# Kernel optimization log

Hardware: AMD Instinct MI355X
Metric: run time of the kernel (lower is better)

The kernel has to match this reference:

```python
import jax, jax.numpy as jnp
import numpy as np

B, T, N, D, H, MH = 4, 16, 128, 16, 64, 128  # batch, timesteps, nodes, n_in_node, n_hid, msg_hid


def setup_inputs() -> dict:
    key = jax.random.key(0)
    ks = jax.random.split(key, 24)
    s = 0.1
    inp = {
        'A': jax.random.uniform(ks[0], (B, N, N), dtype=jnp.float32),
        'X': jax.random.normal(ks[1], (B, T, N, D), dtype=jnp.float32),
        'W_msg1': s * jax.random.normal(ks[2], (2 * H, MH), dtype=jnp.float32),
        'b_msg1': s * jax.random.normal(ks[3], (MH,), dtype=jnp.float32),
        'W_msg2': s * jax.random.normal(ks[4], (MH, H), dtype=jnp.float32),
        'b_msg2': s * jax.random.normal(ks[5], (H,), dtype=jnp.float32),
        'W_ir': s * jax.random.normal(ks[6], (D, H), dtype=jnp.float32),
        'b_ir': s * jax.random.normal(ks[7], (H,), dtype=jnp.float32),
        'W_ii': s * jax.random.normal(ks[8], (D, H), dtype=jnp.float32),
        'b_ii': s * jax.random.normal(ks[9], (H,), dtype=jnp.float32),
        'W_in': s * jax.random.normal(ks[10], (D, H), dtype=jnp.float32),
        'b_in': s * jax.random.normal(ks[11], (H,), dtype=jnp.float32),
        'W_hr': s * jax.random.normal(ks[12], (H, H), dtype=jnp.float32),
        'W_hi': s * jax.random.normal(ks[13], (H, H), dtype=jnp.float32),
        'W_hh': s * jax.random.normal(ks[14], (H, H), dtype=jnp.float32),
        'W_o1': s * jax.random.normal(ks[15], (H, H), dtype=jnp.float32),
        'b_o1': s * jax.random.normal(ks[16], (H,), dtype=jnp.float32),
        'W_o2': s * jax.random.normal(ks[17], (H, H), dtype=jnp.float32),
        'b_o2': s * jax.random.normal(ks[18], (H,), dtype=jnp.float32),
        'W_o3': s * jax.random.normal(ks[19], (H, D), dtype=jnp.float32),
        'b_o3': s * jax.random.normal(ks[20], (D,), dtype=jnp.float32),
        'log_sigma': jnp.log(jnp.float32(0.1)),
    }
    return inp


def reference(A, X, W_msg1, b_msg1, W_msg2, b_msg2, W_ir, b_ir, W_ii, b_ii,
              W_in, b_in, W_hr, W_hi, W_hh, W_o1, b_o1, W_o2, b_o2, W_o3,
              b_o3, log_sigma):
    Bv, Tv, Nv, Dv = X.shape
    Hv = W_hr.shape[0]
    # project_adjacency: symmetrize, zero diag, clamp to [0,1]
    A = (A + jnp.swapaxes(A, -1, -2)) * 0.5
    A = A * (1.0 - jnp.eye(Nv, dtype=A.dtype))
    A = jnp.clip(A, 0.0, 1.0)
    # split msg_fc1 into sender / receiver halves (cat([senders, receivers]) @ W)
    W1s, W1r = W_msg1[:Hv], W_msg1[Hv:]

    def step(carry, xs):
        hidden, total = carry
        x_t, x_next = xs  # [B,N,D]
        # message passing on hidden state: msg1[b,i,j] = tanh(h_i@W1s + h_j@W1r + b)
        hs = hidden @ W1s                      # [B,N,MH] sender part
        hr = hidden @ W1r + b_msg1             # [B,N,MH] receiver part
        m1 = jnp.tanh(hs[:, :, None, :] + hr[:, None, :, :])  # [B,N,N,MH]
        msg = jnp.tanh(m1 @ W_msg2 + b_msg2)   # [B,N,N,H]
        # weight by soft adjacency, sum over senders i -> agg at receiver j
        agg = jnp.einsum('bij,bijh->bjh', A, msg)  # [B,N,H]
        # GRU-style gating
        r = jax.nn.sigmoid(x_t @ W_ir + b_ir + agg @ W_hr)
        i = jax.nn.sigmoid(x_t @ W_ii + b_ii + agg @ W_hi)
        n = jnp.tanh(x_t @ W_in + b_in + r * (agg @ W_hh))
        hidden_new = (1.0 - i) * n + i * hidden
        # output MLP with residual
        p1 = jax.nn.relu(hidden_new @ W_o1 + b_o1)
        p2 = jax.nn.relu(p1 @ W_o2 + b_o2)
        pred = x_t + (p2 @ W_o3 + b_o3)
        # gaussian log-likelihood
        sigma = jnp.exp(log_sigma)
        mse = jnp.sum((x_next - pred) ** 2)
        const = Nv * Dv * Bv * jnp.log(sigma * jnp.sqrt(2.0 * jnp.pi))
        total = total - (mse / (2.0 * sigma ** 2) + const)
        return (hidden_new, total), pred

    hidden0 = jnp.zeros((Bv, Nv, Hv), dtype=X.dtype)
    xs = (jnp.swapaxes(X[:, :-1], 0, 1), jnp.swapaxes(X[:, 1:], 0, 1))  # time-major
    (_, loglik), preds = jax.lax.scan(step, (hidden0, jnp.float32(0.0)), xs)
    X_pred = jnp.swapaxes(preds, 0, 1)  # [B, T-1, N, D]
    return X_pred, loglik
```

## Files before the change

kernel.cpp:

```cpp
#include <hip/hip_runtime.h>

#define NBLK 512
#define CSCALE 2.8853900817779268f

#define OFF_HS   0
#define OFF_PART 65536
#define OFF_SYNC 66048
#define OFF_BF   85248

#define SYNC_ROOT 15360
#define SYNC_FLAG 17280

#define BW2F  0
#define BWIR  8192
#define BWII  9216
#define BWIN  10240
#define BWHR  11264
#define BWHI  15360
#define BWHH  19456
#define BWO1  23552
#define BWO2  27648
#define BWO3  31744
#define BW1S  32768
#define BW1RT 49152

#define INIT_TOTAL (32768 + 19200 + 49152 + 8192)

typedef __attribute__((ext_vector_type(8))) __bf16 bf16x8;
typedef __attribute__((ext_vector_type(4))) float f32x4;
union frag_u { bf16x8 v; unsigned short s[8]; int4 q; };
union ldu { int4 q; unsigned short s[8]; unsigned u[4]; };

__device__ __forceinline__ unsigned short f2b(float x) {
  unsigned int u = __float_as_uint(x);
  u += 0x7fffu + ((u >> 16) & 1u);
  return (unsigned short)(u >> 16);
}
__device__ __forceinline__ float b2f(unsigned short u) {
  return __uint_as_float(((unsigned int)u) << 16);
}
__device__ __forceinline__ float fast_tanh(float x) {
  float e = __builtin_amdgcn_exp2f(x * CSCALE);
  return 1.0f - 2.0f * __builtin_amdgcn_rcpf(e + 1.0f);
}
__device__ __forceinline__ float tanh_pre(float x) {
  float e = __builtin_amdgcn_exp2f(x);
  return 1.0f - 2.0f * __builtin_amdgcn_rcpf(e + 1.0f);
}
__device__ __forceinline__ float fast_sigmoid(float x) {
  float e = __builtin_amdgcn_exp2f(x * -1.4426950408889634f);
  return __builtin_amdgcn_rcpf(1.0f + e);
}
__device__ __forceinline__ unsigned pack_bf2(float lo, float hi) {
  unsigned a = __float_as_uint(lo) + 0x8000u;
  unsigned b = __float_as_uint(hi) + 0x8000u;
  return __builtin_amdgcn_perm(b, a, 0x07060302u);
}
__device__ __forceinline__ void st_coh_u32(unsigned* p, unsigned v) {
  __hip_atomic_store(p, v, __ATOMIC_RELAXED, __HIP_MEMORY_SCOPE_AGENT);
}

__global__ void init_kernel(const float* __restrict__ W_msg2,
                            const float* __restrict__ W_ir, const float* __restrict__ W_ii,
                            const float* __restrict__ W_in,
                            const float* __restrict__ W_hr, const float* __restrict__ W_hi,
                            const float* __restrict__ W_hh,
                            const float* __restrict__ W_o1, const float* __restrict__ W_o2,
                            const float* __restrict__ W_o3,
                            const float* __restrict__ W_msg1, float* __restrict__ ws) {
  int idx = blockIdx.x * 256 + threadIdx.x;
  unsigned short* bw = (unsigned short*)(ws + OFF_BF);
  if (idx < 32768) { ws[OFF_HS + idx] = 0.0f; return; }
  idx -= 32768;
  if (idx < 19200) { ((int*)(ws + OFF_SYNC))[idx] = 0; return; }
  idx -= 19200;
  if (idx < 8192) {
    int f = idx >> 9, l = (idx >> 3) & 63, jj = idx & 7;
    int kc = f >> 2, nt = f & 3;
    int k = kc * 32 + ((l >> 4) << 3) + jj;
    int n = (nt << 4) + (l & 15);
    bw[BW2F + idx] = f2b(W_msg2[k * 64 + n] * CSCALE);
    return;
  }
  idx -= 8192;
  if (idx < 1024) { bw[BWIR + idx] = f2b(W_ir[idx]); return; }
  idx -= 1024;
  if (idx < 1024) { bw[BWII + idx] = f2b(W_ii[idx]); return; }
  idx -= 1024;
  if (idx < 1024) { bw[BWIN + idx] = f2b(W_in[idx]); return; }
  idx -= 1024;
  if (idx < 4096) { bw[BWHR + idx] = f2b(W_hr[idx]); return; }
  idx -= 4096;
  if (idx < 4096) { bw[BWHI + idx] = f2b(W_hi[idx]); return; }
  idx -= 4096;
  if (idx < 4096) { bw[BWHH + idx] = f2b(W_hh[idx]); return; }
  idx -= 4096;
  if (idx < 4096) { bw[BWO1 + idx] = f2b(W_o1[idx]); return; }
  idx -= 4096;
  if (idx < 4096) { bw[BWO2 + idx] = f2b(W_o2[idx]); return; }
  idx -= 4096;
  if (idx < 1024) { bw[BWO3 + idx] = f2b(W_o3[idx]); return; }
  idx -= 1024;
  if (idx < 16384) { bw[BW1S + idx] = f2b(W_msg1[idx]); return; }
  idx -= 16384;
  if (idx < 8192) {
    int m = idx >> 6, h = idx & 63;
    bw[BW1RT + idx] = f2b(W_msg1[(64 + h) * 128 + m]);
    return;
  }
}

__launch_bounds__(512, 4)
__global__ void step_all_kernel(const float* __restrict__ A, const float* __restrict__ X,
                                const float* __restrict__ b_msg1, const float* __restrict__ b_msg2,
                                const float* __restrict__ b_ir, const float* __restrict__ b_ii,
                                const float* __restrict__ b_in,
                                const float* __restrict__ b_o1, const float* __restrict__ b_o2,
                                const float* __restrict__ b_o3,
                                float* __restrict__ ws, float* __restrict__ out) {
  const int tid = threadIdx.x;
  const int bj = blockIdx.x;
  const int b = (bj >> 6) & 3;
  const int j = (bj & 63) | ((bj >> 8) << 6);
  const int row = (b << 7) + j;
  const int wave = tid >> 6, lane = tid & 63;
  const unsigned short* bw = (const unsigned short*)(ws + OFF_BF);
  unsigned short* hs16 = (unsigned short*)(ws + OFF_HS);
  int* sync = (int*)(ws + OFF_SYNC);

  __shared__ __align__(16) unsigned short lds_bf[8192];
  __shared__ __align__(16) unsigned short lds_gate_t[12288];
  __shared__ __align__(16) unsigned short lds_w1t[8192];
  __shared__ __align__(16) unsigned short lds_xw[3072];
  __shared__ __align__(16) float sh_hr[128];
  __shared__ __align__(16) float sh_Ar[128];
  __shared__ __align__(16) float sh_aggw[8][64];
  __shared__ __align__(16) float sh_agg[64];
  __shared__ __align__(16) float sh_xall[256];
  __shared__ __align__(16) float sh_hid[64];
  __shared__ __align__(16) float sh_hist[960];
  __shared__ __align__(16) float sh_pre[8][64];
  __shared__ int sh_w01;

  {
    const int4* src = (const int4*)bw;
    int4* dst = (int4*)lds_bf;
    for (int i = tid; i < 1024; i += 512) dst[i] = src[i];
  }
  for (int i = tid; i < 12288; i += 512) {
    int g = i >> 12, r = i & 4095, c = r >> 8, rem = r & 255, h = rem >> 2, s = rem & 3;
    lds_gate_t[i] = bw[BWHR + (g << 12) + (((c << 2) + s) << 6) + h];
  }
  for (int i = tid; i < 8192; i += 512) {
    int c = i >> 9, rem = i & 511, m = rem >> 2, s = rem & 3;
    lds_w1t[i] = bw[BW1S + (((c << 2) + s) << 7) + m];
  }
  for (int i = tid; i < 3072; i += 512) lds_xw[i] = bw[BWIR + i];
  if (tid < 256) {
    int t0 = tid >> 4, d = tid & 15;
    sh_xall[tid] = X[(((b << 4) + t0) << 11) + (j << 4) + d];
  }
  if (tid < 128) {
    float a1 = A[(b << 14) + (j << 7) + tid];
    float a2 = A[(b << 14) + (tid << 7) + j];
    float v = 0.5f * (a1 + a2);
    v = (tid == j) ? 0.0f : v;
    sh_Ar[tid] = fminf(fmaxf(v, 0.0f), 1.0f);
    sh_hr[tid] = b_msg1[tid] * CSCALE;
  } else if (tid < 192) {
    sh_hid[tid - 128] = 0.0f;
  }
  if (tid == 0) sh_w01 = 0;

  float b2v[4];
#pragma unroll
  for (int nt = 0; nt < 4; ++nt) b2v[nt] = b_msg2[nt * 16 + (lane & 15)] * CSCALE;
  float my_bias = 0.0f;
  if (wave == 0) my_bias = b_ir[lane];
  else if (wave == 1) my_bias = b_ii[lane];
  else if (wave == 3) my_bias = b_in[lane];
  const float bm1a = b_msg1[lane], bm1b = b_msg1[lane + 64];
  const float bo1 = b_o1[lane], bo2 = b_o2[lane];
  const float bo3 = (lane < 16) ? b_o3[lane] : 0.0f;
  float macc = 0.0f;

  const int lane15 = lane & 15;
  const int k0 = (lane >> 4) << 3;
  __syncthreads();

  for (int t = 0; t < 15; ++t) {
    const int par = t & 1;
    const unsigned short* hs_cur = hs16 + par * 65536;
    unsigned short* hs_nxt = hs16 + (par ^ 1) * 65536;

    ldu va[4];
    {
      const unsigned short* p0 = hs_cur + (((b << 7) + (wave << 4) + lane15) << 7) + k0;
      asm volatile(
          "global_load_dwordx4 %0, %4, off sc0 sc1\n\t"
          "global_load_dwordx4 %1, %4, off offset:64 sc0 sc1\n\t"
          "global_load_dwordx4 %2, %4, off offset:128 sc0 sc1\n\t"
          "global_load_dwordx4 %3, %4, off offset:192 sc0 sc1\n\t"
          "s_waitcnt vmcnt(0)"
          : "=&v"(va[0].q), "=&v"(va[1].q), "=&v"(va[2].q), "=&v"(va[3].q)
          : "v"(p0)
          : "memory");
    }

    float part[4] = {0.f, 0.f, 0.f, 0.f};
    {
      f32x4 acc[4];
#pragma unroll
      for (int nt = 0; nt < 4; ++nt) acc[nt] = (f32x4){0.f, 0.f, 0.f, 0.f};
#pragma unroll
      for (int kc = 0; kc < 4; ++kc) {
        const ldu& u = va[kc];
        const float* hp = sh_hr + kc * 32 + k0;
        frag_u Af;
        int* ap = (int*)&Af.q;
#pragma unroll
        for (int p = 0; p < 4; ++p) {
          unsigned w = u.u[p];
          float x0 = __uint_as_float(w << 16) + hp[2 * p];
          float x1 = __uint_as_float(w & 0xffff0000u) + hp[2 * p + 1];
          ap[p] = (int)pack_bf2(tanh_pre(x0), tanh_pre(x1));
        }
#pragma unroll
        for (int nt = 0; nt < 4; ++nt) {
          frag_u Bfr;
          Bfr.q = *(((const int4*)lds_bf) + (((kc << 2) + nt) << 6) + lane);
          acc[nt] = __builtin_amdgcn_mfma_f32_16x16x32_bf16(Af.v, Bfr.v, acc[nt], 0, 0, 0);
        }
      }
      const int ibase = wave << 4;
      float4 aw = *(const float4*)(sh_Ar + ibase + ((lane >> 4) << 2));
#pragma unroll
      for (int r = 0; r < 4; ++r) {
        float wv = (r == 0) ? aw.x : (r == 1) ? aw.y : (r == 2) ? aw.z : aw.w;
#pragma unroll
        for (int nt = 0; nt < 4; ++nt)
          part[nt] += wv * tanh_pre(acc[nt][r] + b2v[nt]);
      }
    }
#pragma unroll
    for (int nt = 0; nt < 4; ++nt) {
      part[nt] += __shfl_xor(part[nt], 16);
      part[nt] += __shfl_xor(part[nt], 32);
    }
    if (lane < 16) {
#pragma unroll
      for (int nt = 0; nt < 4; ++nt) sh_aggw[wave][nt * 16 + lane] = part[nt];
    }
    __syncthreads();
    if (tid < 64) {
      float s = 0.0f;
#pragma unroll
      for (int w = 0; w < 8; ++w) s += sh_aggw[w][tid];
      sh_agg[tid] = s;
    }
    __syncthreads();

    if (wave < 4) {
      float s = 0.0f;
      if (wave != 2) {
        s = my_bias;
        const int g = (wave == 3) ? 2 : wave;
        const float* xr = sh_xall + (t << 4);
#pragma unroll
        for (int d = 0; d < 16; ++d) s += xr[d] * b2f(lds_xw[(g << 10) + (d << 6) + lane]);
      }
      if (wave != 3) {
        const ushort4* gp = ((const ushort4*)lds_gate_t) + (wave << 10) + lane;
        const float4* ag = (const float4*)sh_agg;
        float a0 = s, a1 = 0.f, a2 = 0.f, a3 = 0.f;
#pragma unroll
        for (int c = 0; c < 16; ++c) {
          ushort4 wv = gp[c << 6];
          float4 av = ag[c];
          a0 += av.x * b2f(wv.x); a1 += av.y * b2f(wv.y);
          a2 += av.z * b2f(wv.z); a3 += av.w * b2f(wv.w);
        }
        s = (a0 + a1) + (a2 + a3);
      }
      sh_pre[wave][lane] = s;
    }
    __syncthreads();
    if (tid < 64) {
      float r  = fast_sigmoid(sh_pre[0][tid]);
      float ig = fast_sigmoid(sh_pre[1][tid]);
      float n  = fast_tanh(sh_pre[3][tid] + r * sh_pre[2][tid]);
      float hnew = (1.0f - ig) * n + ig * sh_hid[tid];
      sh_hid[tid] = hnew;
      sh_hist[t * 64 + tid] = hnew;
    }
    __syncthreads();

    if (t < 14) {
      if (wave <= 1) {
        const int m = tid;
        const ushort4* wp = ((const ushort4*)lds_w1t) + m;
        const float4* h4 = (const float4*)sh_hid;
        float a0 = 0.f, a1 = 0.f, a2 = 0.f, a3 = 0.f;
#pragma unroll
        for (int c = 0; c < 16; ++c) {
          ushort4 wv = wp[c << 7];
          float4 hv = h4[c];
          a0 += hv.x * b2f(wv.x); a1 += hv.y * b2f(wv.y);
          a2 += hv.z * b2f(wv.z); a3 += hv.w * b2f(wv.w);
        }
        float s = ((a0 + a1) + (a2 + a3)) * CSCALE;
        float hi = __shfl_down(s, 1);
        if (!(lane & 1))
          st_coh_u32((unsigned*)hs_nxt + (row << 6) + (m >> 1), pack_bf2(s, hi));
        asm volatile("s_waitcnt vmcnt(0)" ::: "memory");
        if (lane == 0) atomicAdd(&sh_w01, 1);
        if (wave == 0 && lane == 0) {
          const int tgt = t + 1;
          while (__hip_atomic_load(&sh_w01, __ATOMIC_RELAXED, __HIP_MEMORY_SCOPE_WORKGROUP) < 2 * tgt) {}
          const int bt = b * 15 + t;
          int* leaf = sync + ((bt << 3) + (j & 7)) * 32;
          int* root = sync + SYNC_ROOT + bt * 32;
          int* flag = sync + SYNC_FLAG + bt * 32;
          int r = __hip_atomic_fetch_add(leaf, 1, __ATOMIC_RELAXED, __HIP_MEMORY_SCOPE_AGENT);
          if (r == 15) {
            int r2 = __hip_atomic_fetch_add(root, 1, __ATOMIC_RELAXED, __HIP_MEMORY_SCOPE_AGENT);
            if (r2 == 7)
              __hip_atomic_store(flag, 1, __ATOMIC_RELAXED, __HIP_MEMORY_SCOPE_AGENT);
          }
          while (__hip_atomic_load(flag, __ATOMIC_RELAXED, __HIP_MEMORY_SCOPE_AGENT) == 0)
            __builtin_amdgcn_s_sleep(1);
        }
      } else if (wave == 2) {
        const int4* wp1 = (const int4*)(bw + BW1RT + (lane << 6));
        const int4* wp2 = (const int4*)(bw + BW1RT + ((lane + 64) << 6));
        const float4* h4 = (const float4*)sh_hid;
        float s1a = bm1a, s1b = 0.f, s2a = bm1b, s2b = 0.f;
#pragma unroll
        for (int c = 0; c < 8; ++c) {
          ldu u1, u2; u1.q = wp1[c]; u2.q = wp2[c];
          float4 h0 = h4[2 * c], h1 = h4[2 * c + 1];
          s1a += h0.x * b2f(u1.s[0]); s1b += h0.y * b2f(u1.s[1]);
          s1a += h0.z * b2f(u1.s[2]); s1b += h0.w * b2f(u1.s[3]);
          s1a += h1.x * b2f(u1.s[4]); s1b += h1.y * b2f(u1.s[5]);
          s1a += h1.z * b2f(u1.s[6]); s1b += h1.w * b2f(u1.s[7]);
          s2a += h0.x * b2f(u2.s[0]); s2b += h0.y * b2f(u2.s[1]);
          s2a += h0.z * b2f(u2.s[2]); s2b += h0.w * b2f(u2.s[3]);
          s2a += h1.x * b2f(u2.s[4]); s2b += h1.y * b2f(u2.s[5]);
          s2a += h1.z * b2f(u2.s[6]); s2b += h1.w * b2f(u2.s[7]);
        }
        sh_hr[lane] = (s1a + s1b) * CSCALE;
        sh_hr[lane + 64] = (s2a + s2b) * CSCALE;
      }
    }
    __syncthreads();
  }

  for (int i = tid; i < 8192; i += 512) {
    int o = i >> 12, r = i & 4095, c = r >> 8, rem = r & 255, h = rem >> 2, s = rem & 3;
    lds_gate_t[i] = bw[BWO1 + (o << 12) + (((c << 2) + s) << 6) + h];
  }
  for (int i = tid; i < 1024; i += 512) {
    int c = i >> 6, rem = i & 63, d = rem >> 2, s = rem & 3;
    lds_gate_t[8192 + i] = bw[BWO3 + (((c << 2) + s) << 4) + d];
  }
  __syncthreads();

#pragma unroll
  for (int it = 0; it < 2; ++it) {
    const int tt = wave + (it << 3);
    if (tt >= 15) continue;
    const float4* h4 = (const float4*)(sh_hist + tt * 64);
    {
      const ushort4* r1 = ((const ushort4*)lds_gate_t) + lane;
      float a0 = bo1, a1 = 0.f, a2 = 0.f, a3 = 0.f;
#pragma unroll
      for (int c = 0; c < 16; ++c) {
        ushort4 wv = r1[c << 6]; float4 hv = h4[c];
        a0 += hv.x * b2f(wv.x); a1 += hv.y * b2f(wv.y);
        a2 += hv.z * b2f(wv.z); a3 += hv.w * b2f(wv.w);
      }
      sh_pre[wave][lane] = fmaxf((a0 + a1) + (a2 + a3), 0.0f);
    }
    {
      const ushort4* r2 = ((const ushort4*)lds_gate_t) + 1024 + lane;
      const float4* p4 = (const float4*)sh_pre[wave];
      float a0 = bo2, a1 = 0.f, a2 = 0.f, a3 = 0.f;
#pragma unroll
      for (int c = 0; c < 16; ++c) {
        ushort4 wv = r2[c << 6]; float4 pv = p4[c];
        a0 += pv.x * b2f(wv.x); a1 += pv.y * b2f(wv.y);
        a2 += pv.z * b2f(wv.z); a3 += pv.w * b2f(wv.w);
      }
      sh_aggw[wave][lane] = fmaxf((a0 + a1) + (a2 + a3), 0.0f);
    }
    if (lane < 16) {
      const ushort4* r3 = ((const ushort4*)lds_gate_t) + 2048 + lane;
      const float4* q4 = (const float4*)sh_aggw[wave];
      float a0 = bo3, a1 = 0.f, a2 = 0.f, a3 = 0.f;
#pragma unroll
      for (int c = 0; c < 16; ++c) {
        ushort4 wv = r3[c << 4]; float4 qv = q4[c];
        a0 += qv.x * b2f(wv.x); a1 += qv.y * b2f(wv.y);
        a2 += qv.z * b2f(wv.z); a3 += qv.w * b2f(wv.w);
      }
      float pred = sh_xall[(tt << 4) + lane] + (a0 + a1) + (a2 + a3);
      out[((b * 15 + tt) * 128 + j) * 16 + lane] = pred;
      float d = sh_xall[((tt + 1) << 4) + lane] - pred;
      macc += d * d;
    }
  }
  macc += __shfl_xor(macc, 1);
  macc += __shfl_xor(macc, 2);
  macc += __shfl_xor(macc, 4);
  macc += __shfl_xor(macc, 8);
  __syncthreads();
  if (lane == 0) sh_agg[wave] = macc;
  __syncthreads();
  if (tid == 0) {
    float s = 0.0f;
#pragma unroll
    for (int w = 0; w < 8; ++w) s += sh_agg[w];
    ws[OFF_PART + bj] = s;
  }
}

__global__ void final_kernel(const float* __restrict__ log_sigma, const float* __restrict__ ws,
                             float* __restrict__ out) {
  __shared__ float red[256];
  const int tid = threadIdx.x;
  red[tid] = ws[OFF_PART + tid] + ws[OFF_PART + 256 + tid];
  __syncthreads();
  if (tid == 0) {
    float mse = 0.0f;
    for (int i = 0; i < 256; ++i) mse += red[i];
    float sigma = expf(log_sigma[0]);
    float cst = 8192.0f * logf(sigma * sqrtf(6.2831853071795864f));
    out[122880] = -(mse / (2.0f * sigma * sigma) + 15.0f * cst);
  }
}

extern "C" void kernel_launch(void* const* d_in, const int* in_sizes, int n_in,
                              void* d_out, int out_size, void* d_ws, size_t ws_size,
                              hipStream_t stream) {
  (void)in_sizes; (void)n_in; (void)out_size; (void)ws_size;
  const float* A      = (const float*)d_in[0];
  const float* X      = (const float*)d_in[1];
  const float* W_msg1 = (const float*)d_in[2];
  const float* b_msg1 = (const float*)d_in[3];
  const float* W_msg2 = (const float*)d_in[4];
  const float* b_msg2 = (const float*)d_in[5];
  const float* W_ir   = (const float*)d_in[6];
  const float* b_ir   = (const float*)d_in[7];
  const float* W_ii   = (const float*)d_in[8];
  const float* b_ii   = (const float*)d_in[9];
  const float* W_in   = (const float*)d_in[10];
  const float* b_in   = (const float*)d_in[11];
  const float* W_hr   = (const float*)d_in[12];
  const float* W_hi   = (const float*)d_in[13];
  const float* W_hh   = (const float*)d_in[14];
  const float* W_o1   = (const float*)d_in[15];
  const float* b_o1   = (const float*)d_in[16];
  const float* W_o2   = (const float*)d_in[17];
  const float* b_o2   = (const float*)d_in[18];
  const float* W_o3   = (const float*)d_in[19];
  const float* b_o3   = (const float*)d_in[20];
  const float* log_sigma = (const float*)d_in[21];
  float* ws  = (float*)d_ws;
  float* out = (float*)d_out;

  init_kernel<<<(INIT_TOTAL + 255) / 256, 256, 0, stream>>>(
      W_msg2, W_ir, W_ii, W_in, W_hr, W_hi, W_hh, W_o1, W_o2, W_o3, W_msg1, ws);
  step_all_kernel<<<NBLK, 512, 0, stream>>>(A, X, b_msg1, b_msg2, b_ir, b_ii, b_in,
                                            b_o1, b_o2, b_o3, ws, out);
  final_kernel<<<1, 256, 0, stream>>>(log_sigma, ws, out);
}
```

Baseline: 244.4 us.

## Replace per-step tree barrier with per-row progress flags and full hidden history

Drops the two-level atomic counter barrier between timesteps. Each block now publishes a per-row step counter, and before reading, each wave polls only the 16 rows it consumes. The ping-pong hidden buffer becomes a full per-timestep history, so a fast block can no longer overwrite data that slower blocks still read. The aim is to remove global barrier latency and allow blocks to drift, at the cost of more workspace and polling traffic.

```diff
diff --git a/kernel.cpp b/kernel.cpp
--- a/kernel.cpp
+++ b/kernel.cpp
@@ -4,12 +4,9 @@
 #define CSCALE 2.8853900817779268f
 
 #define OFF_HS   0
-#define OFF_PART 65536
-#define OFF_SYNC 66048
-#define OFF_BF   85248
-
-#define SYNC_ROOT 15360
-#define SYNC_FLAG 17280
+#define OFF_PART 491520
+#define OFF_SYNC 492032
+#define OFF_BF   492544
 
 #define BW2F  0
 #define BWIR  8192
@@ -24,7 +21,7 @@
 #define BW1S  32768
 #define BW1RT 49152
 
-#define INIT_TOTAL (32768 + 19200 + 49152 + 8192)
+#define INIT_TOTAL (32768 + 512 + 49152 + 8192)
 
 typedef __attribute__((ext_vector_type(8))) __bf16 bf16x8;
 typedef __attribute__((ext_vector_type(4))) float f32x4;
@@ -57,6 +54,9 @@
   return __builtin_amdgcn_perm(b, a, 0x07060302u);
 }
 __device__ __forceinline__ void st_coh_u32(unsigned* p, unsigned v) {
+  __hip_atomic_store(p, v, __ATOMIC_RELAXED, __HIP_MEMORY_SCOPE_AGENT);
+}
+__device__ __forceinline__ void st_coh_i32(int* p, int v) {
   __hip_atomic_store(p, v, __ATOMIC_RELAXED, __HIP_MEMORY_SCOPE_AGENT);
 }
 
@@ -72,8 +72,8 @@
   unsigned short* bw = (unsigned short*)(ws + OFF_BF);
   if (idx < 32768) { ws[OFF_HS + idx] = 0.0f; return; }
   idx -= 32768;
-  if (idx < 19200) { ((int*)(ws + OFF_SYNC))[idx] = 0; return; }
-  idx -= 19200;
+  if (idx < 512) { ((int*)(ws + OFF_SYNC))[idx] = 0; return; }
+  idx -= 512;
   if (idx < 8192) {
     int f = idx >> 9, l = (idx >> 3) & 63, jj = idx & 7;
     int kc = f >> 2, nt = f & 3;
@@ -126,7 +126,7 @@
   const int wave = tid >> 6, lane = tid & 63;
   const unsigned short* bw = (const unsigned short*)(ws + OFF_BF);
   unsigned short* hs16 = (unsigned short*)(ws + OFF_HS);
-  int* sync = (int*)(ws + OFF_SYNC);
+  int* flags = (int*)(ws + OFF_SYNC);
 
   __shared__ __align__(16) unsigned short lds_bf[8192];
   __shared__ __align__(16) unsigned short lds_gate_t[12288];
@@ -189,9 +189,19 @@
   __syncthreads();
 
   for (int t = 0; t < 15; ++t) {
-    const int par = t & 1;
-    const unsigned short* hs_cur = hs16 + par * 65536;
-    unsigned short* hs_nxt = hs16 + (par ^ 1) * 65536;
+    const unsigned short* hs_cur = hs16 + t * 65536;
+    unsigned short* hs_nxt = hs16 + (t + 1) * 65536;
+
+    if (t > 0) {
+      const int* fp = flags + (b << 7) + (wave << 4) + lane15;
+      int fv;
+      for (;;) {
+        asm volatile("global_load_dword %0, %1, off sc0 sc1\n\ts_waitcnt vmcnt(0)"
+                     : "=v"(fv) : "v"(fp) : "memory");
+        if (!__any(fv < t)) break;
+        __builtin_amdgcn_s_sleep(1);
+      }
+    }
 
     ldu va[4];
     {
@@ -317,18 +327,7 @@
         if (wave == 0 && lane == 0) {
           const int tgt = t + 1;
           while (__hip_atomic_load(&sh_w01, __ATOMIC_RELAXED, __HIP_MEMORY_SCOPE_WORKGROUP) < 2 * tgt) {}
-          const int bt = b * 15 + t;
-          int* leaf = sync + ((bt << 3) + (j & 7)) * 32;
-          int* root = sync + SYNC_ROOT + bt * 32;
-          int* flag = sync + SYNC_FLAG + bt * 32;
-          int r = __hip_atomic_fetch_add(leaf, 1, __ATOMIC_RELAXED, __HIP_MEMORY_SCOPE_AGENT);
-          if (r == 15) {
-            int r2 = __hip_atomic_fetch_add(root, 1, __ATOMIC_RELAXED, __HIP_MEMORY_SCOPE_AGENT);
-            if (r2 == 7)
-              __hip_atomic_store(flag, 1, __ATOMIC_RELAXED, __HIP_MEMORY_SCOPE_AGENT);
-          }
-          while (__hip_atomic_load(flag, __ATOMIC_RELAXED, __HIP_MEMORY_SCOPE_AGENT) == 0)
-            __builtin_amdgcn_s_sleep(1);
+          st_coh_i32(flags + row, tgt);
         }
       } else if (wave == 2) {
         const int4* wp1 = (const int4*)(bw + BW1RT + (lane << 6));
```

Result: slower. 264.9 us (+8.4%).
